# Performance work log

Measured on AMD Instinct MI355X. Metric: run time of the kernel, lower is better.

## Reference

```python
import jax, jax.numpy as jnp
import numpy as np

PARA_CH = 256
FEATURE_CH = 256
PI = 3.14159  # matches the literal in the torch source


def _linear_params(key, fan_in, fan_out):
    kw, kb = jax.random.split(key)
    bound = 1.0 / np.sqrt(fan_in)
    W = jax.random.uniform(kw, (fan_in, fan_out), minval=-bound, maxval=bound, dtype=jnp.float32)
    b = jax.random.uniform(kb, (fan_out,), minval=-bound, maxval=bound, dtype=jnp.float32)
    return W, b


def setup_inputs() -> dict:
    key = jax.random.key(0)
    ks = jax.random.split(key, 6)
    feature_map = jax.random.normal(ks[0], (4, FEATURE_CH, 128, 128), dtype=jnp.float32)
    para_code = jax.random.normal(ks[1], (4, PARA_CH), dtype=jnp.float32)
    W1, b1 = _linear_params(ks[2], PARA_CH, PARA_CH)
    Ws, bs = _linear_params(ks[3], PARA_CH, FEATURE_CH)
    Wr, br = _linear_params(ks[4], PARA_CH, FEATURE_CH)
    Wt, bt = _linear_params(ks[5], PARA_CH, 2 * FEATURE_CH)
    return {"feature_map": feature_map, "para_code": para_code,
            "W1": W1, "b1": b1, "Ws": Ws, "bs": bs,
            "Wr": Wr, "br": br, "Wt": Wt, "bt": bt}


def _coord_1d(n):
    # align_corners=True-style normalized coordinates, as in make_coordinate_grid_3d
    return 2.0 * (jnp.arange(n, dtype=jnp.float32) / (n - 1)) - 1.0


def _trilinear_sample_zeros(vol, gx, gy, gz):
    """F.grid_sample 5D equivalent: mode='bilinear' (trilinear), padding_mode='zeros',
    align_corners=False. vol: [B,D,H,W] (channel dim of size 1 squeezed out);
    gx,gy,gz: [B,Do,Ho,Wo] normalized coords. Returns [B,Do,Ho,Wo]."""
    B, D, H, W = vol.shape
    ix = ((gx + 1.0) * W - 1.0) * 0.5
    iy = ((gy + 1.0) * H - 1.0) * 0.5
    iz = ((gz + 1.0) * D - 1.0) * 0.5
    x0f, y0f, z0f = jnp.floor(ix), jnp.floor(iy), jnp.floor(iz)
    wx, wy, wz = ix - x0f, iy - y0f, iz - z0f
    x0 = x0f.astype(jnp.int32); x1 = x0 + 1
    y0 = y0f.astype(jnp.int32); y1 = y0 + 1
    z0 = z0f.astype(jnp.int32); z1 = z0 + 1
    vflat = vol.reshape(B, -1)

    def gather(zi, yi, xi):
        valid = (zi >= 0) & (zi < D) & (yi >= 0) & (yi < H) & (xi >= 0) & (xi < W)
        zc = jnp.clip(zi, 0, D - 1)
        yc = jnp.clip(yi, 0, H - 1)
        xc = jnp.clip(xi, 0, W - 1)
        flat = (zc * H + yc) * W + xc  # [B,Do,Ho,Wo]
        v = jnp.take_along_axis(vflat, flat.reshape(B, -1), axis=1).reshape(flat.shape)
        return jnp.where(valid, v, 0.0)

    out = (gather(z0, y0, x0) * (1 - wz) * (1 - wy) * (1 - wx)
           + gather(z0, y0, x1) * (1 - wz) * (1 - wy) * wx
           + gather(z0, y1, x0) * (1 - wz) * wy * (1 - wx)
           + gather(z0, y1, x1) * (1 - wz) * wy * wx
           + gather(z1, y0, x0) * wz * (1 - wy) * (1 - wx)
           + gather(z1, y0, x1) * wz * (1 - wy) * wx
           + gather(z1, y1, x0) * wz * wy * (1 - wx)
           + gather(z1, y1, x1) * wz * wy * wx)
    return out


def reference(feature_map, para_code, W1, b1, Ws, bs, Wr, br, Wt, bt):
    B, C, H, W = feature_map.shape  # C == feature_ch == depth of 3D grid
    p = jax.nn.relu(para_code @ W1 + b1)                      # [B, para_ch]
    scale = jax.nn.sigmoid(p @ Ws + bs) * 2.0                 # [B, C]
    angle = jnp.tanh(p @ Wr + br) * PI                        # [B, C]
    translation = jnp.tanh(p @ Wt + bt).reshape(B, C, 2)      # [B, C, 2]
    ca, sa = jnp.cos(angle), jnp.sin(angle)
    # rotation matrix [[cos, -sin], [sin, cos]] per (batch, channel)
    rot = jnp.stack([jnp.stack([ca, -sa], -1), jnp.stack([sa, ca], -1)], -2)  # [B,C,2,2]

    x = _coord_1d(W)  # [W]
    y = _coord_1d(H)  # [H]
    z = _coord_1d(C)  # [C] (depth == channel dim)
    grid_xy = jnp.stack(jnp.broadcast_arrays(x[None, None, :], y[None, :, None]), -1)  # [1,H,W,2] -> broadcast to [C,H,W,2]
    grid_xy = jnp.broadcast_to(grid_xy, (C, H, W, 2))

    # per-pixel affine transform: rot @ [x,y] * scale + trans
    trans_grid = jnp.einsum('bcij,chwj->bchwi', rot, grid_xy)
    trans_grid = trans_grid * scale[:, :, None, None, None] + translation[:, :, None, None, :]
    gx = trans_grid[..., 0]
    gy = trans_grid[..., 1]
    gz = jnp.broadcast_to(z[None, :, None, None], (B, C, H, W))

    return _trilinear_sample_zeros(feature_map, gx, gy, gz)  # [B,C,H,W]
```

## Files before the change

kernel.cpp:

```cpp
#include <hip/hip_runtime.h>
#include <math.h>

#define BATCH 4
#define CH    256
#define HH    128
#define WW    128
#define PC    256
#define PI_F  3.14159f
#define PLANE (HH * WW)

#define PSTRIDE 134
#define PROWS   131
#define BUFSZ   (PROWS * PSTRIDE)

__device__ __forceinline__ void barrier_lds() {
    asm volatile("s_waitcnt lgkmcnt(0)\n\ts_barrier" ::: "memory");
}

struct Stage { float4 a[4]; float4 b[4]; };

__device__ __forceinline__ Stage stage_load(const float* __restrict__ pl0,
                                            const float* __restrict__ pl1, int t) {
    Stage s;
#pragma unroll
    for (int j = 0; j < 4; ++j) {
        const int f = 4 * (t + 1024 * j);
        s.a[j] = *(const float4*)(pl0 + f);
        s.b[j] = *(const float4*)(pl1 + f);
    }
    return s;
}

__device__ __forceinline__ void stage_store_pad(float* __restrict__ buf, const Stage& s,
                                                float wz0, float wz1, int t) {
#pragma unroll
    for (int j = 0; j < 4; ++j) {
        const int f = 4 * (t + 1024 * j);
        const int y = f >> 7, x = f & (WW - 1);
        float* p = &buf[(y + 1) * PSTRIDE + (x + 1)];
        p[0] = fmaf(wz0, s.a[j].x, wz1 * s.b[j].x);
        p[1] = fmaf(wz0, s.a[j].y, wz1 * s.b[j].y);
        p[2] = fmaf(wz0, s.a[j].z, wz1 * s.b[j].z);
        p[3] = fmaf(wz0, s.a[j].w, wz1 * s.b[j].w);
    }
}

__global__ __launch_bounds__(1024, 8)
void adaat_fused_kernel(const float* __restrict__ fm,
                        const float* __restrict__ pc,
                        const float* __restrict__ W1, const float* __restrict__ b1,
                        const float* __restrict__ Ws, const float* __restrict__ bs,
                        const float* __restrict__ Wr, const float* __restrict__ br,
                        const float* __restrict__ Wt, const float* __restrict__ bt,
                        float* __restrict__ out) {
    __shared__ float  lds[BUFSZ];
    __shared__ float  red[1024];
    __shared__ float  p_sh[PC];
    __shared__ float  sh_head[4];
    __shared__ float4 sh_par;

    const int t = threadIdx.x;

    const int bid = blockIdx.x;
    const int lc  = ((bid & 7) << 7) | (bid >> 3);
    const int b   = lc >> 8;
    const int c   = lc & (CH - 1);

    const float* base = fm + (size_t)b * (CH * PLANE);
    const float  iz = (256.0f / 255.0f) * (float)c - 0.5f;
    const float  zf = floorf(iz);
    const float  fz = iz - zf;
    const int    z0 = (int)zf;
    const float  w0 = (z0 >= 0)     ? (1.0f - fz) : 0.0f;
    const float  w1 = (z0 + 1 < CH) ? fz          : 0.0f;
    const float* pl0 = base + (size_t)max(z0, 0)          * PLANE;
    const float* pl1 = base + (size_t)min(z0 + 1, CH - 1) * PLANE;

    Stage s = stage_load(pl0, pl1, t);

#pragma unroll
    for (int i = 0; i < 18; ++i) {
        const int idx = t + 1024 * i;
        if (idx < BUFSZ) lds[idx] = 0.0f;
    }

    {
        const int jj = t & 255, kk = t >> 8;
        const float* pcb = pc + b * PC + kk * 64;
        const float* w   = W1 + (kk * 64) * PC + jj;
        float acc = 0.0f;
#pragma unroll 8
        for (int i = 0; i < 64; ++i)
            acc = fmaf(pcb[i], w[i * PC], acc);
        red[t] = acc;
    }
    barrier_lds();
    if (t < 256)
        p_sh[t] = fmaxf(red[t] + red[256 + t] + red[512 + t] + red[768 + t] + b1[t], 0.0f);
    barrier_lds();

    stage_store_pad(lds, s, w0, w1, t);

    const int wv = t >> 6, l = t & 63;
    if (wv < 4) {
        const float* wp; int stride;
        if      (wv == 0) { wp = Ws + c;               stride = PC;     }
        else if (wv == 1) { wp = Wr + c;               stride = PC;     }
        else              { wp = Wt + 2 * c + (wv == 3); stride = 2 * PC; }
        float dot = 0.0f;
#pragma unroll
        for (int m = 0; m < 4; ++m) {
            const int k = l + 64 * m;
            dot = fmaf(p_sh[k], wp[(size_t)k * stride], dot);
        }
#pragma unroll
        for (int off = 32; off >= 1; off >>= 1)
            dot += __shfl_xor(dot, off, 64);
        if (l == 0) sh_head[wv] = dot;
    }
    barrier_lds();

    if (t == 0) {
        const float s2  = 2.0f / (1.0f + expf(-(sh_head[0] + bs[c])));
        const float ang = tanhf(sh_head[1] + br[c]) * PI_F;
        float sa, ca;
        sincosf(ang, &sa, &ca);
        const float A  = s2 * ca, B = s2 * sa;
        const float Tx = tanhf(sh_head[2] + bt[2 * c]);
        const float Ty = tanhf(sh_head[3] + bt[2 * c + 1]);
        sh_par = make_float4(A * (128.0f / 127.0f),
                             B * (128.0f / 127.0f),
                             64.0f * (Tx - A + B) + 64.5f,
                             64.0f * (Ty - A - B) + 64.5f);
    }
    barrier_lds();

    {
        const float4 P  = sh_par;
        const float  cA = P.x, cB = P.y;
        float* outp = out + (size_t)lc * PLANE;
        const float xf0 = (float)l;
        float rowf = (float)(wv * 8);
#pragma unroll 2
        for (int r = 0; r < 8; ++r) {
            const float bx = fmaf(-cB, rowf, P.z);
            const float by = fmaf( cA, rowf, P.w);
            float* orow = outp + (wv * 8 + r) * WW;
#pragma unroll
            for (int h = 0; h < 2; ++h) {
                const float xf  = xf0 + 64.0f * h;
                const float ix  = fmaf(cA, xf, bx);
                const float iy  = fmaf(cB, xf, by);
                const float xc  = fminf(fmaxf(ix, 0.0f), 129.99f);
                const float yc  = fminf(fmaxf(iy, 0.0f), 129.99f);
                const float x0f = floorf(xc), y0f = floorf(yc);
                const float fx  = xc - x0f,   fy  = yc - y0f;
                const int   a   = (int)y0f * PSTRIDE + (int)x0f;
                const float v00 = lds[a],           v01 = lds[a + 1];
                const float v10 = lds[a + PSTRIDE], v11 = lds[a + PSTRIDE + 1];
                const float h0  = fmaf(fx, v01 - v00, v00);
                const float h1  = fmaf(fx, v11 - v10, v10);
                orow[h * 64 + l] = fmaf(fy, h1 - h0, h0);
            }
            rowf += 1.0f;
        }
    }
}

extern "C" void kernel_launch(void* const* d_in, const int* in_sizes, int n_in,
                              void* d_out, int out_size, void* d_ws, size_t ws_size,
                              hipStream_t stream) {
    const float* feature_map = (const float*)d_in[0];
    const float* para_code   = (const float*)d_in[1];
    const float* W1 = (const float*)d_in[2];
    const float* b1 = (const float*)d_in[3];
    const float* Ws = (const float*)d_in[4];
    const float* bs = (const float*)d_in[5];
    const float* Wr = (const float*)d_in[6];
    const float* br = (const float*)d_in[7];
    const float* Wt = (const float*)d_in[8];
    const float* bt = (const float*)d_in[9];

    adaat_fused_kernel<<<BATCH * CH, 1024, 0, stream>>>(
        feature_map, para_code, W1, b1, Ws, bs, Wr, br, Wt, bt, (float*)d_out);
}
```

Before: 156.8 us.

## Hoist per-channel parameter MLP into separate kernel and zero only LDS border

```diff
diff --git a/kernel.cpp b/kernel.cpp
--- a/kernel.cpp
+++ b/kernel.cpp
@@ -12,6 +12,7 @@
 #define PSTRIDE 134
 #define PROWS   131
 #define BUFSZ   (PROWS * PSTRIDE)
+#define NBORDER 1170
 
 __device__ __forceinline__ void barrier_lds() {
     asm volatile("s_waitcnt lgkmcnt(0)\n\ts_barrier" ::: "memory");
@@ -45,19 +46,70 @@
     }
 }
 
+__global__ __launch_bounds__(1024)
+void adaat_params_kernel(const float* __restrict__ pc,
+                         const float* __restrict__ W1, const float* __restrict__ b1,
+                         const float* __restrict__ Ws, const float* __restrict__ bs,
+                         const float* __restrict__ Wr, const float* __restrict__ br,
+                         const float* __restrict__ Wt, const float* __restrict__ bt,
+                         float4* __restrict__ par) {
+    __shared__ float red[1024];
+    __shared__ float p_sh[PC];
+    __shared__ float hd[4][PC];
+
+    const int t = threadIdx.x;
+    const int b = blockIdx.x;
+
+    {
+        const int jj = t & 255, kk = t >> 8;
+        const float* pcb = pc + b * PC + kk * 64;
+        const float* w   = W1 + (kk * 64) * PC + jj;
+        float acc = 0.0f;
+#pragma unroll 8
+        for (int i = 0; i < 64; ++i)
+            acc = fmaf(pcb[i], w[i * PC], acc);
+        red[t] = acc;
+    }
+    __syncthreads();
+    if (t < 256)
+        p_sh[t] = fmaxf(red[t] + red[256 + t] + red[512 + t] + red[768 + t] + b1[t], 0.0f);
+    __syncthreads();
+
+    {
+        const int c = t & 255, h = t >> 8;
+        const float* wp; int stride;
+        if      (h == 0) { wp = Ws + c;                stride = PC;     }
+        else if (h == 1) { wp = Wr + c;                stride = PC;     }
+        else             { wp = Wt + 2 * c + (h == 3); stride = 2 * PC; }
+        float dot = 0.0f;
+#pragma unroll 8
+        for (int k = 0; k < PC; ++k)
+            dot = fmaf(p_sh[k], wp[(size_t)k * stride], dot);
+        hd[h][c] = dot;
+    }
+    __syncthreads();
+
+    if (t < 256) {
+        const int c = t;
+        const float s2  = 2.0f / (1.0f + expf(-(hd[0][c] + bs[c])));
+        const float ang = tanhf(hd[1][c] + br[c]) * PI_F;
+        float sa, ca;
+        sincosf(ang, &sa, &ca);
+        const float A  = s2 * ca, B = s2 * sa;
+        const float Tx = tanhf(hd[2][c] + bt[2 * c]);
+        const float Ty = tanhf(hd[3][c] + bt[2 * c + 1]);
+        par[b * 256 + c] = make_float4(A * (128.0f / 127.0f),
+                                       B * (128.0f / 127.0f),
+                                       64.0f * (Tx - A + B) + 64.5f,
+                                       64.0f * (Ty - A - B) + 64.5f);
+    }
+}
+
 __global__ __launch_bounds__(1024, 8)
 void adaat_fused_kernel(const float* __restrict__ fm,
-                        const float* __restrict__ pc,
-                        const float* __restrict__ W1, const float* __restrict__ b1,
-                        const float* __restrict__ Ws, const float* __restrict__ bs,
-                        const float* __restrict__ Wr, const float* __restrict__ br,
-                        const float* __restrict__ Wt, const float* __restrict__ bt,
+                        const float4* __restrict__ par,
                         float* __restrict__ out) {
-    __shared__ float  lds[BUFSZ];
-    __shared__ float  red[1024];
-    __shared__ float  p_sh[PC];
-    __shared__ float  sh_head[4];
-    __shared__ float4 sh_par;
+    __shared__ float lds[BUFSZ];
 
     const int t = threadIdx.x;
 
@@ -78,65 +130,30 @@
 
     Stage s = stage_load(pl0, pl1, t);
 
-#pragma unroll
-    for (int i = 0; i < 18; ++i) {
-        const int idx = t + 1024 * i;
-        if (idx < BUFSZ) lds[idx] = 0.0f;
-    }
+    const float4 P = par[lc];
+
+#pragma unroll
+    for (int i = t; i < NBORDER; i += 1024) {
+        int row, col;
+        if (i < 402) {
+            row = i / 134;
+            if (row == 1) row = 129; else if (row == 2) row = 130;
+            col = i % 134;
+        } else {
+            const int j = i - 402;
+            row = 1 + j / 6;
+            const int cs = j % 6;
+            col = (cs == 0) ? 0 : 128 + cs;
+        }
+        lds[row * PSTRIDE + col] = 0.0f;
+    }
+
+    stage_store_pad(lds, s, w0, w1, t);
+
+    barrier_lds();
 
     {
-        const int jj = t & 255, kk = t >> 8;
-        const float* pcb = pc + b * PC + kk * 64;
-        const float* w   = W1 + (kk * 64) * PC + jj;
-        float acc = 0.0f;
-#pragma unroll 8
-        for (int i = 0; i < 64; ++i)
-            acc = fmaf(pcb[i], w[i * PC], acc);
-        red[t] = acc;
-    }
-    barrier_lds();
-    if (t < 256)
-        p_sh[t] = fmaxf(red[t] + red[256 + t] + red[512 + t] + red[768 + t] + b1[t], 0.0f);
-    barrier_lds();
-
-    stage_store_pad(lds, s, w0, w1, t);
-
-    const int wv = t >> 6, l = t & 63;
-    if (wv < 4) {
-        const float* wp; int stride;
-        if      (wv == 0) { wp = Ws + c;               stride = PC;     }
-        else if (wv == 1) { wp = Wr + c;               stride = PC;     }
-        else              { wp = Wt + 2 * c + (wv == 3); stride = 2 * PC; }
-        float dot = 0.0f;
-#pragma unroll
-        for (int m = 0; m < 4; ++m) {
-            const int k = l + 64 * m;
-            dot = fmaf(p_sh[k], wp[(size_t)k * stride], dot);
-        }
-#pragma unroll
-        for (int off = 32; off >= 1; off >>= 1)
-            dot += __shfl_xor(dot, off, 64);
-        if (l == 0) sh_head[wv] = dot;
-    }
-    barrier_lds();
-
-    if (t == 0) {
-        const float s2  = 2.0f / (1.0f + expf(-(sh_head[0] + bs[c])));
-        const float ang = tanhf(sh_head[1] + br[c]) * PI_F;
-        float sa, ca;
-        sincosf(ang, &sa, &ca);
-        const float A  = s2 * ca, B = s2 * sa;
-        const float Tx = tanhf(sh_head[2] + bt[2 * c]);
-        const float Ty = tanhf(sh_head[3] + bt[2 * c + 1]);
-        sh_par = make_float4(A * (128.0f / 127.0f),
-                             B * (128.0f / 127.0f),
-                             64.0f * (Tx - A + B) + 64.5f,
-                             64.0f * (Ty - A - B) + 64.5f);
-    }
-    barrier_lds();
-
-    {
-        const float4 P  = sh_par;
+        const int    wv = t >> 6, l = t & 63;
         const float  cA = P.x, cB = P.y;
         float* outp = out + (size_t)lc * PLANE;
         const float xf0 = (float)l;
@@ -181,6 +198,11 @@
     const float* Wt = (const float*)d_in[8];
     const float* bt = (const float*)d_in[9];
 
+    float4* par = (float4*)d_ws;
+
+    adaat_params_kernel<<<BATCH, 1024, 0, stream>>>(
+        para_code, W1, b1, Ws, bs, Wr, br, Wt, bt, par);
+
     adaat_fused_kernel<<<BATCH * CH, 1024, 0, stream>>>(
-        feature_map, para_code, W1, b1, Ws, bs, Wr, br, Wt, bt, (float*)d_out);
-}
+        feature_map, par, (float*)d_out);
+}
```

After: 161.9 us. +3.3%, slower.
